# Kernel tuning notes

Hardware: AMD Instinct MI355X
Metric: run time of the kernel (lower is better)

Reference implementation:

```python
import jax, jax.numpy as jnp
import numpy as np


def setup_inputs() -> dict:
    key = jax.random.key(0)
    k1, _ = jax.random.split(key)
    B, S, V = 32, 8, 128000
    logits = jax.random.normal(k1, (B, S, V), dtype=jnp.float32)
    temperature = jnp.ones((1,), dtype=jnp.float32)  # broadcasts over last axis like as_tensor
    return {"logits": logits, "temperature": temperature}


def reference(logits, temperature):
    # eval-mode path with temperature: scale, normalize, multinomial-sample.
    # torch.multinomial(probs, 1) == categorical sampling; in JAX the efficient
    # equivalent is the fused Gumbel-max via jax.random.categorical, which never
    # materializes normalized probabilities.
    scaled = logits / temperature                      # [B, S, V]
    logp = jax.nn.log_softmax(scaled, axis=-1)         # logits - logsumexp (single stable pass)
    key = jax.random.key(42)                           # fixed sampling key
    samples = jax.random.categorical(key, logp, axis=-1)  # [B, S] int32
    return samples
```

## Files before the change

### kernel.cpp

```cpp
#include <hip/hip_runtime.h>
#include <stdint.h>
#include <math.h>


constexpr int V = 128000;
constexpr int NROWS = 256;
constexpr int TPB = 256;
constexpr int SPLITQ = 25;

__device__ __forceinline__ uint32_t rotl_(uint32_t x, uint32_t r) {
#if __has_builtin(__builtin_rotateleft32)
  return __builtin_rotateleft32(x, r);
#else
  return (x << r) | (x >> (32u - r));
#endif
}

__device__ __forceinline__ uint32_t threefry_xor_pre(uint32_t x1 ) {
  uint32_t x0;
  x0 = x1;            x1 = rotl_(x1, 13) ^ x0;
  x0 += x1;           x1 = rotl_(x1, 15) ^ x0;
  x0 += x1;           x1 = rotl_(x1, 26) ^ x0;
  x0 += x1;           x1 = rotl_(x1,  6) ^ x0;
  x1 += 0x1BD11BF1u;  x0 = x0 + 42u + x1;
                      x1 = rotl_(x1, 17) ^ x0;
  x0 += x1;           x1 = rotl_(x1, 29) ^ x0;
  x0 += x1;           x1 = rotl_(x1, 16) ^ x0;
  x0 += x1;           x1 = rotl_(x1, 24) ^ x0;
  x1 += 2u;           x0 = x0 + 0x1BD11BF0u + x1;
                      x1 = rotl_(x1, 13) ^ x0;
  x0 += x1;           x1 = rotl_(x1, 15) ^ x0;
  x0 += x1;           x1 = rotl_(x1, 26) ^ x0;
  x0 += x1;           x1 = rotl_(x1,  6) ^ x0;
  x1 += 45u;          x0 = x0 + x1;
                      x1 = rotl_(x1, 17) ^ x0;
  x0 += x1;           x1 = rotl_(x1, 29) ^ x0;
  x0 += x1;           x1 = rotl_(x1, 16) ^ x0;
  x0 += x1;           x1 = rotl_(x1, 24) ^ x0;
  x1 += 0x1BD11BF4u;  x0 = x0 + 42u + x1;
                      x1 = rotl_(x1, 13) ^ x0;
  x0 += x1;           x1 = rotl_(x1, 15) ^ x0;
  x0 += x1;           x1 = rotl_(x1, 26) ^ x0;
  x0 += x1;           x1 = rotl_(x1,  6) ^ x0;
  return (x0 + 0x1BD11BF0u) ^ (x1 + 5u);
}

__device__ __forceinline__ uint32_t mant_pack(uint32_t bits) {
#if __has_builtin(__builtin_amdgcn_alignbit)
  return __builtin_amdgcn_alignbit(127u, bits, 9u);
#else
  return (bits >> 9) | 0x3f800000u;
#endif
}

template <int SPLIT>
__global__ __launch_bounds__(TPB) void CategoricalSampler_stage1(
    const float* __restrict__ logits, const float* __restrict__ temp,
    float2* __restrict__ ws) {
  constexpr int SEG = V / SPLIT;
  constexpr int J = SEG / (TPB * 4);
  const int b   = blockIdx.x;
  const int row = b / SPLIT;
  const int seg = b - row * SPLIT;
  const int t   = threadIdx.x;
  const float scale = 1.4426950408889634f / temp[0];
  const int segbase = seg * SEG;
  const float4* rp4 = reinterpret_cast<const float4*>(logits + (size_t)row * V + segbase);
  const uint32_t cb42 = (uint32_t)row * (uint32_t)V + (uint32_t)segbase
                      + (uint32_t)(t * 4) + 42u;

  float4 L[J];
#pragma unroll
  for (int j = 0; j < J; ++j) L[j] = rp4[j * TPB + t];

  float best = -INFINITY;
  int bestCode = 0;

#pragma unroll
  for (int j = 0; j < J; ++j) {
    const uint32_t c0 = cb42 + (uint32_t)(j * TPB * 4);
#pragma unroll
    for (int k = 0; k < 4; ++k) {
      const uint32_t bits = threefry_xor_pre(c0 + (uint32_t)k);
      const float u  = __uint_as_float(mant_pack(bits)) - 1.0f;
      const float s1 = __log2f(u);
      const float s2 = __log2f(-s1);
      const float lk = (k == 0) ? L[j].x : (k == 1) ? L[j].y : (k == 2) ? L[j].z : L[j].w;
      const float val = fmaf(lk, scale, -s2);
      if (val > best) { best = val; bestCode = j * 4 + k; }
    }
  }

  int bestIdx = segbase + (bestCode >> 2) * (TPB * 4) + (t << 2) + (bestCode & 3);

#pragma unroll
  for (int off = 32; off > 0; off >>= 1) {
    const float ov = __shfl_down(best, off);
    const int   oi = __shfl_down(bestIdx, off);
    if (ov > best || (ov == best && oi < bestIdx)) { best = ov; bestIdx = oi; }
  }

  __shared__ float sv[TPB / 64];
  __shared__ int   si[TPB / 64];
  const int wid = t >> 6;
  if ((t & 63) == 0) { sv[wid] = best; si[wid] = bestIdx; }
  __syncthreads();
  if (t == 0) {
    float bv = sv[0]; int bi = si[0];
#pragma unroll
    for (int w = 1; w < TPB / 64; ++w) {
      if (sv[w] > bv || (sv[w] == bv && si[w] < bi)) { bv = sv[w]; bi = si[w]; }
    }
    ws[b] = make_float2(bv, __int_as_float(bi));
  }
}

template <int SPLIT>
__global__ __launch_bounds__(64) void CategoricalSampler_stage2(
    const float2* __restrict__ ws, int* __restrict__ out) {
  const int r = blockIdx.x;
  const int l = threadIdx.x;
  float best = -INFINITY;
  int bestIdx = 0x7FFFFFFF;
  if (l < SPLIT) {
    const float2 p = ws[r * SPLIT + l];
    best = p.x; bestIdx = __float_as_int(p.y);
  }
#pragma unroll
  for (int off = 32; off > 0; off >>= 1) {
    const float ov = __shfl_down(best, off);
    const int   oi = __shfl_down(bestIdx, off);
    if (ov > best || (ov == best && oi < bestIdx)) { best = ov; bestIdx = oi; }
  }
  if (l == 0) out[r] = bestIdx;
}

extern "C" void kernel_launch(void* const* d_in, const int* in_sizes, int n_in,
                              void* d_out, int out_size, void* d_ws, size_t ws_size,
                              hipStream_t stream) {
  const float* logits = (const float*)d_in[0];
  const float* temp   = (const float*)d_in[1];
  int* out = (int*)d_out;
  float2* ws = (float2*)d_ws;
  if (ws_size >= (size_t)NROWS * SPLITQ * sizeof(float2)) {
    CategoricalSampler_stage1<SPLITQ><<<NROWS * SPLITQ, TPB, 0, stream>>>(logits, temp, ws);
    CategoricalSampler_stage2<SPLITQ><<<NROWS, 64, 0, stream>>>(ws, out);
  } else {
    CategoricalSampler_stage1<5><<<NROWS * 5, TPB, 0, stream>>>(logits, temp, ws);
    CategoricalSampler_stage2<5><<<NROWS, 64, 0, stream>>>(ws, out);
  }
}
```

Baseline: 70.15 us.

## Batch threefry over 8 lanes, stream loads, recompute argmax index lazily

Threefry hashing is interleaved across 8 counters at a time to expose instruction-level parallelism. Logits are loaded two float4s per iteration instead of all being preloaded into registers, and launch bounds now request 8 waves per SIMD. The inner loop tracks only the best float4 group using fmax; the element index within that group is recovered afterwards by recomputing four Gumbel values. This trades a small amount of extra compute and a reload for fewer compares and less register pressure.

```diff
diff --git a/kernel.cpp b/kernel.cpp
--- a/kernel.cpp
+++ b/kernel.cpp
@@ -16,33 +16,40 @@
 #endif
 }
 
-__device__ __forceinline__ uint32_t threefry_xor_pre(uint32_t x1 ) {
-  uint32_t x0;
-  x0 = x1;            x1 = rotl_(x1, 13) ^ x0;
-  x0 += x1;           x1 = rotl_(x1, 15) ^ x0;
-  x0 += x1;           x1 = rotl_(x1, 26) ^ x0;
-  x0 += x1;           x1 = rotl_(x1,  6) ^ x0;
-  x1 += 0x1BD11BF1u;  x0 = x0 + 42u + x1;
-                      x1 = rotl_(x1, 17) ^ x0;
-  x0 += x1;           x1 = rotl_(x1, 29) ^ x0;
-  x0 += x1;           x1 = rotl_(x1, 16) ^ x0;
-  x0 += x1;           x1 = rotl_(x1, 24) ^ x0;
-  x1 += 2u;           x0 = x0 + 0x1BD11BF0u + x1;
-                      x1 = rotl_(x1, 13) ^ x0;
-  x0 += x1;           x1 = rotl_(x1, 15) ^ x0;
-  x0 += x1;           x1 = rotl_(x1, 26) ^ x0;
-  x0 += x1;           x1 = rotl_(x1,  6) ^ x0;
-  x1 += 45u;          x0 = x0 + x1;
-                      x1 = rotl_(x1, 17) ^ x0;
-  x0 += x1;           x1 = rotl_(x1, 29) ^ x0;
-  x0 += x1;           x1 = rotl_(x1, 16) ^ x0;
-  x0 += x1;           x1 = rotl_(x1, 24) ^ x0;
-  x1 += 0x1BD11BF4u;  x0 = x0 + 42u + x1;
-                      x1 = rotl_(x1, 13) ^ x0;
-  x0 += x1;           x1 = rotl_(x1, 15) ^ x0;
-  x0 += x1;           x1 = rotl_(x1, 26) ^ x0;
-  x0 += x1;           x1 = rotl_(x1,  6) ^ x0;
-  return (x0 + 0x1BD11BF0u) ^ (x1 + 5u);
+#define TF_ROUND(r) \
+  _Pragma("unroll") \
+  for (int i = 0; i < N; ++i) { x0[i] += x1[i]; x1[i] = rotl_(x1[i], (r)) ^ x0[i]; }
+
+template <int N>
+__device__ __forceinline__ void threefry_xor_batch(const uint32_t* c, uint32_t* out) {
+  uint32_t x0[N], x1[N];
+#pragma unroll
+  for (int i = 0; i < N; ++i) {
+    x1[i] = c[i]; x0[i] = x1[i]; x1[i] = rotl_(x1[i], 13) ^ x0[i];
+  }
+  TF_ROUND(15) TF_ROUND(26) TF_ROUND(6)
+#pragma unroll
+  for (int i = 0; i < N; ++i) {
+    x1[i] += 0x1BD11BF1u; x0[i] = x0[i] + 42u + x1[i]; x1[i] = rotl_(x1[i], 17) ^ x0[i];
+  }
+  TF_ROUND(29) TF_ROUND(16) TF_ROUND(24)
+#pragma unroll
+  for (int i = 0; i < N; ++i) {
+    x1[i] += 2u; x0[i] = x0[i] + 0x1BD11BF0u + x1[i]; x1[i] = rotl_(x1[i], 13) ^ x0[i];
+  }
+  TF_ROUND(15) TF_ROUND(26) TF_ROUND(6)
+#pragma unroll
+  for (int i = 0; i < N; ++i) {
+    x1[i] += 45u; x0[i] += x1[i]; x1[i] = rotl_(x1[i], 17) ^ x0[i];
+  }
+  TF_ROUND(29) TF_ROUND(16) TF_ROUND(24)
+#pragma unroll
+  for (int i = 0; i < N; ++i) {
+    x1[i] += 0x1BD11BF4u; x0[i] = x0[i] + 42u + x1[i]; x1[i] = rotl_(x1[i], 13) ^ x0[i];
+  }
+  TF_ROUND(15) TF_ROUND(26) TF_ROUND(6)
+#pragma unroll
+  for (int i = 0; i < N; ++i) out[i] = (x0[i] + 0x1BD11BF0u) ^ (x1[i] + 5u);
 }
 
 __device__ __forceinline__ uint32_t mant_pack(uint32_t bits) {
@@ -53,8 +60,15 @@
 #endif
 }
 
+__device__ __forceinline__ float gval(uint32_t bits, float l, float scale) {
+  const float u  = __uint_as_float(mant_pack(bits)) - 1.0f;
+  const float s1 = __log2f(u);
+  const float s2 = __log2f(-s1);
+  return fmaf(l, scale, -s2);
+}
+
 template <int SPLIT>
-__global__ __launch_bounds__(TPB) void CategoricalSampler_stage1(
+__global__ __launch_bounds__(TPB, 8) void CategoricalSampler_stage1(
     const float* __restrict__ logits, const float* __restrict__ temp,
     float2* __restrict__ ws) {
   constexpr int SEG = V / SPLIT;
@@ -69,49 +83,76 @@
   const uint32_t cb42 = (uint32_t)row * (uint32_t)V + (uint32_t)segbase
                       + (uint32_t)(t * 4) + 42u;
 
-  float4 L[J];
-#pragma unroll
-  for (int j = 0; j < J; ++j) L[j] = rp4[j * TPB + t];
-
   float best = -INFINITY;
-  int bestCode = 0;
+  int bestJ = 0;
 
 #pragma unroll
-  for (int j = 0; j < J; ++j) {
-    const uint32_t c0 = cb42 + (uint32_t)(j * TPB * 4);
+  for (int jb = 0; jb + 2 <= J; jb += 2) {
+    const float4 L0 = rp4[jb * TPB + t];
+    const float4 L1 = rp4[(jb + 1) * TPB + t];
+    uint32_t c[8], bits[8];
 #pragma unroll
     for (int k = 0; k < 4; ++k) {
-      const uint32_t bits = threefry_xor_pre(c0 + (uint32_t)k);
-      const float u  = __uint_as_float(mant_pack(bits)) - 1.0f;
-      const float s1 = __log2f(u);
-      const float s2 = __log2f(-s1);
-      const float lk = (k == 0) ? L[j].x : (k == 1) ? L[j].y : (k == 2) ? L[j].z : L[j].w;
-      const float val = fmaf(lk, scale, -s2);
-      if (val > best) { best = val; bestCode = j * 4 + k; }
+      c[k]     = cb42 + (uint32_t)(jb * TPB * 4 + k);
+      c[4 + k] = cb42 + (uint32_t)((jb + 1) * TPB * 4 + k);
     }
+    threefry_xor_batch<8>(c, bits);
+    const float lv[8] = {L0.x, L0.y, L0.z, L0.w, L1.x, L1.y, L1.z, L1.w};
+    float v[8];
+#pragma unroll
+    for (int i = 0; i < 8; ++i) v[i] = gval(bits[i], lv[i], scale);
+    const float m0 = fmaxf(fmaxf(v[0], v[1]), fmaxf(v[2], v[3]));
+    const float m1 = fmaxf(fmaxf(v[4], v[5]), fmaxf(v[6], v[7]));
+    if (m0 > best) { best = m0; bestJ = jb; }
+    if (m1 > best) { best = m1; bestJ = jb + 1; }
+  }
+  if constexpr (J & 1) {
+    constexpr int j = J - 1;
+    const float4 L0 = rp4[j * TPB + t];
+    uint32_t c[4], bits[4];
+#pragma unroll
+    for (int k = 0; k < 4; ++k) c[k] = cb42 + (uint32_t)(j * TPB * 4 + k);
+    threefry_xor_batch<4>(c, bits);
+    const float lv[4] = {L0.x, L0.y, L0.z, L0.w};
+    float m = -INFINITY;
+#pragma unroll
+    for (int i = 0; i < 4; ++i) m = fmaxf(m, gval(bits[i], lv[i], scale));
+    if (m > best) { best = m; bestJ = j; }
   }
 
-  int bestIdx = segbase + (bestCode >> 2) * (TPB * 4) + (t << 2) + (bestCode & 3);
+  {
+    uint32_t c[4], bits[4];
+#pragma unroll
+    for (int k = 0; k < 4; ++k) c[k] = cb42 + (uint32_t)(bestJ * (TPB * 4) + k);
+    threefry_xor_batch<4>(c, bits);
+    const float4 L = rp4[bestJ * TPB + t];
+    const float r0 = gval(bits[0], L.x, scale);
+    const float r1 = gval(bits[1], L.y, scale);
+    const float r2 = gval(bits[2], L.z, scale);
+    const int kk = (r0 == best) ? 0 : (r1 == best) ? 1 : (r2 == best) ? 2 : 3;
+    const int bestIdx = segbase + bestJ * (TPB * 4) + (t << 2) + kk;
 
+    float bv = best; int bi = bestIdx;
 #pragma unroll
-  for (int off = 32; off > 0; off >>= 1) {
-    const float ov = __shfl_down(best, off);
-    const int   oi = __shfl_down(bestIdx, off);
-    if (ov > best || (ov == best && oi < bestIdx)) { best = ov; bestIdx = oi; }
-  }
+    for (int off = 32; off > 0; off >>= 1) {
+      const float ov = __shfl_down(bv, off);
+      const int   oi = __shfl_down(bi, off);
+      if (ov > bv || (ov == bv && oi < bi)) { bv = ov; bi = oi; }
+    }
 
-  __shared__ float sv[TPB / 64];
-  __shared__ int   si[TPB / 64];
-  const int wid = t >> 6;
-  if ((t & 63) == 0) { sv[wid] = best; si[wid] = bestIdx; }
-  __syncthreads();
-  if (t == 0) {
-    float bv = sv[0]; int bi = si[0];
+    __shared__ float sv[TPB / 64];
+    __shared__ int   si[TPB / 64];
+    const int wid = t >> 6;
+    if ((t & 63) == 0) { sv[wid] = bv; si[wid] = bi; }
+    __syncthreads();
+    if (t == 0) {
+      float fv = sv[0]; int fi = si[0];
 #pragma unroll
-    for (int w = 1; w < TPB / 64; ++w) {
-      if (sv[w] > bv || (sv[w] == bv && si[w] < bi)) { bv = sv[w]; bi = si[w]; }
+      for (int w = 1; w < TPB / 64; ++w) {
+        if (sv[w] > fv || (sv[w] == fv && si[w] < fi)) { fv = sv[w]; fi = si[w]; }
+      }
+      ws[b] = make_float2(fv, __int_as_float(fi));
     }
-    ws[b] = make_float2(bv, __int_as_float(bi));
   }
 }
 
```

New measurement: 77.67 us. +10.7%, slower.

## Skip Gumbel logs for small uniforms with exact max-bound fallback

Applied to the files above, without the earlier changes.

Stage 1 now evaluates the two log2 calls and the compare only when the random bits exceed a threshold B0, so only candidates with a large enough Gumbel noise term are scored. It also tracks the segment maximum of the logits. Stage 2 checks whether the winner clears lmax*scale + 7.44, and if not it recomputes the whole row exactly with one wavefront. This removes most transcendental work in exchange for a data-dependent fallback that is very slow on the rows that hit it, plus streaming the logit loads instead of preloading them into registers.

```diff
diff --git a/kernel.cpp b/kernel.cpp
--- a/kernel.cpp
+++ b/kernel.cpp
@@ -8,6 +8,9 @@
 constexpr int TPB = 256;
 constexpr int SPLITQ = 25;
 
+constexpr uint32_t B0 = 8355054u << 9;
+#define G2TAU 7.44f
+
 __device__ __forceinline__ uint32_t rotl_(uint32_t x, uint32_t r) {
 #if __has_builtin(__builtin_rotateleft32)
   return __builtin_rotateleft32(x, r);
@@ -16,32 +19,32 @@
 #endif
 }
 
-__device__ __forceinline__ uint32_t threefry_xor_pre(uint32_t x1 ) {
-  uint32_t x0;
-  x0 = x1;            x1 = rotl_(x1, 13) ^ x0;
-  x0 += x1;           x1 = rotl_(x1, 15) ^ x0;
-  x0 += x1;           x1 = rotl_(x1, 26) ^ x0;
-  x0 += x1;           x1 = rotl_(x1,  6) ^ x0;
-  x1 += 0x1BD11BF1u;  x0 = x0 + 42u + x1;
-                      x1 = rotl_(x1, 17) ^ x0;
-  x0 += x1;           x1 = rotl_(x1, 29) ^ x0;
-  x0 += x1;           x1 = rotl_(x1, 16) ^ x0;
-  x0 += x1;           x1 = rotl_(x1, 24) ^ x0;
-  x1 += 2u;           x0 = x0 + 0x1BD11BF0u + x1;
-                      x1 = rotl_(x1, 13) ^ x0;
-  x0 += x1;           x1 = rotl_(x1, 15) ^ x0;
-  x0 += x1;           x1 = rotl_(x1, 26) ^ x0;
-  x0 += x1;           x1 = rotl_(x1,  6) ^ x0;
-  x1 += 45u;          x0 = x0 + x1;
-                      x1 = rotl_(x1, 17) ^ x0;
-  x0 += x1;           x1 = rotl_(x1, 29) ^ x0;
-  x0 += x1;           x1 = rotl_(x1, 16) ^ x0;
-  x0 += x1;           x1 = rotl_(x1, 24) ^ x0;
-  x1 += 0x1BD11BF4u;  x0 = x0 + 42u + x1;
-                      x1 = rotl_(x1, 13) ^ x0;
-  x0 += x1;           x1 = rotl_(x1, 15) ^ x0;
-  x0 += x1;           x1 = rotl_(x1, 26) ^ x0;
-  x0 += x1;           x1 = rotl_(x1,  6) ^ x0;
+__device__ __forceinline__ uint32_t threefry_xor_pre(uint32_t c) {
+  uint32_t x1 = rotl_(c, 13) ^ c;
+  uint32_t x0 = c + x1;
+  x1 = rotl_(x1, 15) ^ x0;
+  x0 += x1; x1 = rotl_(x1, 26) ^ x0;
+  x0 += x1; x1 = rotl_(x1,  6) ^ x0;
+  x1 += 0x1BD11BF1u; x0 = x0 + 42u + x1;
+  x1 = rotl_(x1, 17) ^ x0;
+  x0 += x1; x1 = rotl_(x1, 29) ^ x0;
+  x0 += x1; x1 = rotl_(x1, 16) ^ x0;
+  x0 += x1; x1 = rotl_(x1, 24) ^ x0;
+  x1 += 2u; x0 = x0 + 0x1BD11BF0u + x1;
+  x1 = rotl_(x1, 13) ^ x0;
+  x0 += x1; x1 = rotl_(x1, 15) ^ x0;
+  x0 += x1; x1 = rotl_(x1, 26) ^ x0;
+  x0 += x1; x1 = rotl_(x1,  6) ^ x0;
+  x1 += 45u; x0 += x1;
+  x1 = rotl_(x1, 17) ^ x0;
+  x0 += x1; x1 = rotl_(x1, 29) ^ x0;
+  x0 += x1; x1 = rotl_(x1, 16) ^ x0;
+  x0 += x1; x1 = rotl_(x1, 24) ^ x0;
+  x1 += 0x1BD11BF4u; x0 = x0 + 42u + x1;
+  x1 = rotl_(x1, 13) ^ x0;
+  x0 += x1; x1 = rotl_(x1, 15) ^ x0;
+  x0 += x1; x1 = rotl_(x1, 26) ^ x0;
+  x0 += x1; x1 = rotl_(x1,  6) ^ x0;
   return (x0 + 0x1BD11BF0u) ^ (x1 + 5u);
 }
 
@@ -53,10 +56,17 @@
 #endif
 }
 
+__device__ __forceinline__ float gval(uint32_t bits, float l, float scale) {
+  const float u  = __uint_as_float(mant_pack(bits)) - 1.0f;
+  const float s1 = __log2f(u);
+  const float s2 = __log2f(-s1);
+  return fmaf(l, scale, -s2);
+}
+
 template <int SPLIT>
 __global__ __launch_bounds__(TPB) void CategoricalSampler_stage1(
     const float* __restrict__ logits, const float* __restrict__ temp,
-    float2* __restrict__ ws) {
+    float2* __restrict__ ws1, float* __restrict__ wsl) {
   constexpr int SEG = V / SPLIT;
   constexpr int J = SEG / (TPB * 4);
   const int b   = blockIdx.x;
@@ -69,25 +79,23 @@
   const uint32_t cb42 = (uint32_t)row * (uint32_t)V + (uint32_t)segbase
                       + (uint32_t)(t * 4) + 42u;
 
-  float4 L[J];
-#pragma unroll
-  for (int j = 0; j < J; ++j) L[j] = rp4[j * TPB + t];
-
   float best = -INFINITY;
   int bestCode = 0;
+  float lmax = -INFINITY;
 
 #pragma unroll
   for (int j = 0; j < J; ++j) {
+    const float4 L = rp4[j * TPB + t];
+    lmax = fmaxf(lmax, fmaxf(fmaxf(L.x, L.y), fmaxf(L.z, L.w)));
     const uint32_t c0 = cb42 + (uint32_t)(j * TPB * 4);
 #pragma unroll
     for (int k = 0; k < 4; ++k) {
       const uint32_t bits = threefry_xor_pre(c0 + (uint32_t)k);
-      const float u  = __uint_as_float(mant_pack(bits)) - 1.0f;
-      const float s1 = __log2f(u);
-      const float s2 = __log2f(-s1);
-      const float lk = (k == 0) ? L[j].x : (k == 1) ? L[j].y : (k == 2) ? L[j].z : L[j].w;
-      const float val = fmaf(lk, scale, -s2);
-      if (val > best) { best = val; bestCode = j * 4 + k; }
+      if (bits >= B0) {
+        const float lk = (k == 0) ? L.x : (k == 1) ? L.y : (k == 2) ? L.z : L.w;
+        const float val = gval(bits, lk, scale);
+        if (val > best) { best = val; bestCode = j * 4 + k; }
+      }
     }
   }
 
@@ -97,42 +105,72 @@
   for (int off = 32; off > 0; off >>= 1) {
     const float ov = __shfl_down(best, off);
     const int   oi = __shfl_down(bestIdx, off);
+    const float ol = __shfl_down(lmax, off);
     if (ov > best || (ov == best && oi < bestIdx)) { best = ov; bestIdx = oi; }
+    lmax = fmaxf(lmax, ol);
   }
 
   __shared__ float sv[TPB / 64];
   __shared__ int   si[TPB / 64];
+  __shared__ float sl[TPB / 64];
   const int wid = t >> 6;
-  if ((t & 63) == 0) { sv[wid] = best; si[wid] = bestIdx; }
+  if ((t & 63) == 0) { sv[wid] = best; si[wid] = bestIdx; sl[wid] = lmax; }
   __syncthreads();
   if (t == 0) {
-    float bv = sv[0]; int bi = si[0];
+    float fv = sv[0]; int fi = si[0]; float fl = sl[0];
 #pragma unroll
     for (int w = 1; w < TPB / 64; ++w) {
-      if (sv[w] > bv || (sv[w] == bv && si[w] < bi)) { bv = sv[w]; bi = si[w]; }
+      if (sv[w] > fv || (sv[w] == fv && si[w] < fi)) { fv = sv[w]; fi = si[w]; }
+      fl = fmaxf(fl, sl[w]);
     }
-    ws[b] = make_float2(bv, __int_as_float(bi));
+    ws1[b] = make_float2(fv, __int_as_float(fi));
+    wsl[b] = fl;
   }
 }
 
 template <int SPLIT>
 __global__ __launch_bounds__(64) void CategoricalSampler_stage2(
-    const float2* __restrict__ ws, int* __restrict__ out) {
+    const float2* __restrict__ ws1, const float* __restrict__ wsl,
+    const float* __restrict__ logits, const float* __restrict__ temp,
+    int* __restrict__ out) {
   const int r = blockIdx.x;
   const int l = threadIdx.x;
-  float best = -INFINITY;
-  int bestIdx = 0x7FFFFFFF;
+  const float scale = 1.4426950408889634f / temp[0];
+  float best = -INFINITY; int bestIdx = 0x7FFFFFFF; float lmax = -INFINITY;
   if (l < SPLIT) {
-    const float2 p = ws[r * SPLIT + l];
+    const float2 p = ws1[r * SPLIT + l];
     best = p.x; bestIdx = __float_as_int(p.y);
+    lmax = wsl[r * SPLIT + l];
   }
 #pragma unroll
   for (int off = 32; off > 0; off >>= 1) {
     const float ov = __shfl_down(best, off);
     const int   oi = __shfl_down(bestIdx, off);
+    const float ol = __shfl_down(lmax, off);
     if (ov > best || (ov == best && oi < bestIdx)) { best = ov; bestIdx = oi; }
+    lmax = fmaxf(lmax, ol);
   }
-  if (l == 0) out[r] = bestIdx;
+  best = __shfl(best, 0); bestIdx = __shfl(bestIdx, 0); lmax = __shfl(lmax, 0);
+  const float bound = fmaf(lmax, scale, G2TAU);
+  if (best >= bound) {
+    if (l == 0) out[r] = bestIdx;
+    return;
+  }
+  const uint32_t cb42 = (uint32_t)r * (uint32_t)V + 42u;
+  const float* rowp = logits + (size_t)r * V;
+  float fb = -INFINITY; int fi = 0;
+  for (int v = l; v < V; v += 64) {
+    const uint32_t bits = threefry_xor_pre(cb42 + (uint32_t)v);
+    const float val = gval(bits, rowp[v], scale);
+    if (val > fb) { fb = val; fi = v; }
+  }
+#pragma unroll
+  for (int off = 32; off > 0; off >>= 1) {
+    const float ov = __shfl_down(fb, off);
+    const int   oi = __shfl_down(fi, off);
+    if (ov > fb || (ov == fb && oi < fi)) { fb = ov; fi = oi; }
+  }
+  if (l == 0) out[r] = fi;
 }
 
 extern "C" void kernel_launch(void* const* d_in, const int* in_sizes, int n_in,
@@ -141,12 +179,15 @@
   const float* logits = (const float*)d_in[0];
   const float* temp   = (const float*)d_in[1];
   int* out = (int*)d_out;
-  float2* ws = (float2*)d_ws;
-  if (ws_size >= (size_t)NROWS * SPLITQ * sizeof(float2)) {
-    CategoricalSampler_stage1<SPLITQ><<<NROWS * SPLITQ, TPB, 0, stream>>>(logits, temp, ws);
-    CategoricalSampler_stage2<SPLITQ><<<NROWS, 64, 0, stream>>>(ws, out);
+  if (ws_size >= (size_t)NROWS * SPLITQ * (sizeof(float2) + sizeof(float))) {
+    float2* ws1 = (float2*)d_ws;
+    float*  wsl = (float*)(ws1 + NROWS * SPLITQ);
+    CategoricalSampler_stage1<SPLITQ><<<NROWS * SPLITQ, TPB, 0, stream>>>(logits, temp, ws1, wsl);
+    CategoricalSampler_stage2<SPLITQ><<<NROWS, 64, 0, stream>>>(ws1, wsl, logits, temp, out);
   } else {
-    CategoricalSampler_stage1<5><<<NROWS * 5, TPB, 0, stream>>>(logits, temp, ws);
-    CategoricalSampler_stage2<5><<<NROWS, 64, 0, stream>>>(ws, out);
+    float2* ws1 = (float2*)d_ws;
+    float*  wsl = (float*)(ws1 + NROWS * 5);
+    CategoricalSampler_stage1<5><<<NROWS * 5, TPB, 0, stream>>>(logits, temp, ws1, wsl);
+    CategoricalSampler_stage2<5><<<NROWS, 64, 0, stream>>>(ws1, wsl, logits, temp, out);
   }
 }
```

Measured after the change: 67.70 us. 1.04x faster.
